# Kernel optimization log

Hardware: AMD Instinct MI355X
Metric: run time of the kernel (lower is better)

Reference implementation:

```python
import math
import jax, jax.numpy as jnp
import numpy as np

K = 30          # tokens per node (most recent links)
IN_CH = 100     # edge feature dim
HID = 100       # hidden channels
OUT_CH = 100    # output channels
TCH = 100       # temporal encoding dim
N = 50000       # num nodes
E = 800000      # num edges


def setup_inputs() -> dict:
    key = jax.random.key(0)
    ks = jax.random.split(key, 16)
    rn = lambda k, shape, s=0.05: (jax.random.normal(k, shape, jnp.float32) * s)
    return {
        'edge_attr': jax.random.normal(ks[0], (E, IN_CH), jnp.float32),
        'edge_time': jax.random.uniform(ks[1], (E,), jnp.float32),
        'node_batch': jax.random.randint(ks[2], (E,), 0, N, jnp.int32),
        'num_nodes': N,
        'head_w': rn(ks[3], (HID, TCH + IN_CH)), 'head_b': jnp.zeros((HID,), jnp.float32),
        'ln_t_g': jnp.ones((HID,), jnp.float32), 'ln_t_b': jnp.zeros((HID,), jnp.float32),
        'tok1_w': rn(ks[4], (K // 2, K)), 'tok1_b': jnp.zeros((K // 2,), jnp.float32),
        'tok2_w': rn(ks[5], (K, K // 2)), 'tok2_b': jnp.zeros((K,), jnp.float32),
        'ln_c_g': jnp.ones((HID,), jnp.float32), 'ln_c_b': jnp.zeros((HID,), jnp.float32),
        'ch1_w': rn(ks[6], (4 * HID, HID)), 'ch1_b': jnp.zeros((4 * HID,), jnp.float32),
        'ch2_w': rn(ks[7], (HID, 4 * HID)), 'ch2_b': jnp.zeros((HID,), jnp.float32),
        'ln_h_g': jnp.ones((HID,), jnp.float32), 'ln_h_b': jnp.zeros((HID,), jnp.float32),
        'out_w': rn(ks[8], (OUT_CH, HID)), 'out_b': jnp.zeros((OUT_CH,), jnp.float32),
    }


def _layer_norm(x, g, b, eps=1e-5):
    m = x.mean(-1, keepdims=True)
    v = ((x - m) ** 2).mean(-1, keepdims=True)
    return (x - m) * jax.lax.rsqrt(v + eps) * g + b


def _gelu(x):
    return jax.nn.gelu(x, approximate=False)  # torch default GELU is exact erf


def reference(edge_attr, edge_time, node_batch, num_nodes,
              head_w, head_b, ln_t_g, ln_t_b, tok1_w, tok1_b, tok2_w, tok2_b,
              ln_c_g, ln_c_b, ch1_w, ch1_b, ch2_w, ch2_b, ln_h_g, ln_h_b,
              out_w, out_b):
    # TemporalEncoding: cos(t * 1/sqrt(d)**linspace(0, sqrt(d), d))
    sqrt_d = math.sqrt(TCH)
    tw = 1.0 / sqrt_d ** jnp.linspace(0.0, sqrt_d, TCH)          # [TCH]
    time_info = jnp.cos(edge_time[:, None] * tw[None, :])        # [E, TCH]
    h = jnp.concatenate([time_info, edge_attr], axis=1) @ head_w.T + head_b  # [E, HID]

    # stable sort by node, take first K edges per node (PyG to_dense_batch)
    perm = jnp.argsort(node_batch)                               # stable
    nb = node_batch[perm]
    h = h[perm]
    pos = jnp.arange(nb.shape[0]) - jnp.searchsorted(nb, nb, side='left')
    idx = jnp.where(pos < K, nb * K + pos, num_nodes * K)        # overflow row -> garbage
    buf = jnp.zeros((num_nodes * K + 1, HID), h.dtype).at[idx].set(h)
    x = buf[:num_nodes * K].reshape(num_nodes, K, HID)           # [N, K, HID]

    # MLP-mixer (eval mode: dropout is identity)
    ht = _layer_norm(x, ln_t_g, ln_t_b).swapaxes(1, 2)           # [N, HID, K]
    ht = _gelu(ht @ tok1_w.T + tok1_b) @ tok2_w.T + tok2_b       # [N, HID, K]
    h_token = ht.swapaxes(1, 2) + x                              # [N, K, HID]

    hc = _layer_norm(h_token, ln_c_g, ln_c_b)
    hc = _gelu(hc @ ch1_w.T + ch1_b) @ ch2_w.T + ch2_b
    h_channel = hc + h_token                                     # [N, K, HID]

    t = _layer_norm(h_channel, ln_h_g, ln_h_b).mean(axis=1)      # [N, HID]
    return t @ out_w.T + out_b                                   # [N, OUT_CH]
```

## Files before the change

### kernel.cpp

```cpp
#include <hip/hip_runtime.h>
#include <math.h>

#define KTOK 30
#define HIDC 100
#define SBD() __builtin_amdgcn_sched_barrier(0x7F)
#define CEXP 0.33554829241286486f

typedef short s16x8 __attribute__((ext_vector_type(8)));
typedef float f32x4 __attribute__((ext_vector_type(4)));

__device__ __forceinline__ unsigned cvt_pk_bf16(float lo, float hi) {
    unsigned r;
    asm("v_cvt_pk_bf16_f32 %0, %1, %2" : "=v"(r) : "v"(lo), "v"(hi));
    return r;
}
__device__ __forceinline__ unsigned short cvt_bf16(float x) {
    unsigned r;
    asm("v_cvt_pk_bf16_f32 %0, %1, 0" : "=v"(r) : "v"(x));
    return (unsigned short)r;
}
__device__ __forceinline__ float bf2f(unsigned short h) {
    return __uint_as_float(((unsigned)h) << 16);
}
__device__ __forceinline__ float exp2_fast(float x) {
    float r;
    asm("v_exp_f32 %0, %1" : "=v"(r) : "v"(x));
    return r;
}
__device__ __forceinline__ float cos_rev(float rev) {
    float r;
    asm("v_cos_f32 %0, %1" : "=v"(r) : "v"(rev));
    return r;
}
__device__ __forceinline__ unsigned short f2bf(float f) {
    unsigned u = __float_as_uint(f);
    unsigned r = (u + 0x7FFFu + ((u >> 16) & 1u)) >> 16;
    return (unsigned short)r;
}
__device__ __forceinline__ float gelu(float x) {
    float xc = fminf(fmaxf(x, -2.75f), 2.75f);
    float s = xc * xc;
    float q = fmaf(s, -0.00059132f, 0.0132267f);
    q = fmaf(q, s, -0.122945f);
    q = fmaf(q, s, 0.793839f);
    float p = xc * q;
    float t = __builtin_amdgcn_fmed3f(p, -1.0f, 1.0f);
    float hx = 0.5f * x;
    return fmaf(hx, t, hx);
}

__global__ void count_kernel(const int* __restrict__ nb, int* __restrict__ cnt, int E) {
    int e = blockIdx.x * blockDim.x + threadIdx.x;
    if (e < E) atomicAdd(&cnt[nb[e]], 1);
}

__global__ void scanA_kernel(const int* __restrict__ cnt, int* __restrict__ offsets,
                             int* __restrict__ bsum, int n) {
    __shared__ int sd[1024];
    int tid = threadIdx.x;
    int i = blockIdx.x * 1024 + tid;
    int v = (i < n) ? cnt[i] : 0;
    sd[tid] = v;
    __syncthreads();
    for (int off = 1; off < 1024; off <<= 1) {
        int tv = (tid >= off) ? sd[tid - off] : 0;
        __syncthreads();
        sd[tid] += tv;
        __syncthreads();
    }
    if (i < n) offsets[i] = sd[tid] - v;
    if (tid == 1023) bsum[blockIdx.x] = sd[1023];
}

__global__ void scanB_kernel(int* __restrict__ bsum, int nbk) {
    if (threadIdx.x == 0 && blockIdx.x == 0) {
        int run = 0;
        for (int b = 0; b < nbk; b++) { int tv = bsum[b]; bsum[b] = run; run += tv; }
    }
}

__global__ void scanC_kernel(int* __restrict__ offsets, const int* __restrict__ bsum, int n) {
    int i = blockIdx.x * blockDim.x + threadIdx.x;
    if (i < n) offsets[i] += bsum[i >> 10];
}

__global__ void fill_kernel(const int* __restrict__ nb, int* __restrict__ cursor,
                            const int* __restrict__ offsets, int* __restrict__ order, int E) {
    int e = blockIdx.x * blockDim.x + threadIdx.x;
    if (e >= E) return;
    int n = nb[e];
    int p = atomicAdd(&cursor[n], 1);
    order[offsets[n] + p] = e;
}

__global__ void select_kernel(const int* __restrict__ cnt, const int* __restrict__ offsets,
                              const int* __restrict__ order, int* __restrict__ sel, int N) {
    int node = blockIdx.x * blockDim.x + threadIdx.x;
    if (node >= N) return;
    int c = cnt[node];
    int off = offsets[node];
    int top[KTOK];
    int m = 0;
    for (int i = 0; i < c; i++) {
        int e = order[off + i];
        if (m < KTOK) {
            int j = m++;
            while (j > 0 && top[j - 1] > e) { top[j] = top[j - 1]; j--; }
            top[j] = e;
        } else if (e < top[KTOK - 1]) {
            int j = KTOK - 1;
            while (j > 0 && top[j - 1] > e) { top[j] = top[j - 1]; j--; }
            top[j] = e;
        }
    }
    for (int p = 0; p < KTOK; p++) sel[node * KTOK + p] = (p < m) ? top[p] : -1;
}

__global__ void prep_kernel(const float* __restrict__ head_w, const float* __restrict__ ch1_w,
                            const float* __restrict__ ch2_w, const float* __restrict__ tok1_w,
                            const float* __restrict__ tok2_w,
                            const float* __restrict__ ln_c_g, const float* __restrict__ ln_c_b,
                            const float* __restrict__ ch1_b,
                            unsigned short* __restrict__ wf,
                            float* __restrict__ Sg1, float* __restrict__ b1p) {
    int i = blockIdx.x * blockDim.x + threadIdx.x;
    if (i >= 128000) {
        int h = i - 128000;
        if (h < 400) {
            float sg = 0.f, sb = 0.f;
            for (int k = 0; k < 100; k++) {
                float w = ch1_w[h * 100 + k];
                sg += w * ln_c_g[k];
                sb += w * ln_c_b[k];
            }
            Sg1[h] = sg;
            b1p[h] = sb + ch1_b[h];
        }
        return;
    }
    float val = 0.0f;
    if (i < 28672) {
        int ii = i & 7, lane = (i >> 3) & 63, rest = i >> 9;
        int nt = rest % 7, kt = rest / 7;
        int k = kt * 32 + ((lane >> 4) << 3) + ii;
        int n = nt * 16 + (lane & 15);
        if (k < 200 && n < 100) val = head_w[n * 200 + k];
    } else if (i < 79872) {
        int j = i - 28672;
        int ii = j & 7, lane = (j >> 3) & 63, rest = j >> 9;
        int nt = rest % 25, kt = rest / 25;
        int k = kt * 32 + ((lane >> 4) << 3) + ii;
        int n = nt * 16 + (lane & 15);
        if (k < 100) val = ch1_w[n * 100 + k] * ln_c_g[k];
    } else if (i < 126464) {
        int j = i - 79872;
        int ii = j & 7, lane = (j >> 3) & 63, rest = j >> 9;
        int nt = rest % 7, kt = rest / 7;
        int k = kt * 32 + ((lane >> 4) << 3) + ii;
        int n = nt * 16 + (lane & 15);
        if (k < 400 && n < 100) val = ch2_w[n * 400 + k];
    } else if (i < 126976) {
        int j = i - 126464;
        int ii = j & 7, lane = (j >> 3) & 63;
        int k = ((lane >> 4) << 3) + ii;
        int n = lane & 15;
        if (k < 30 && n < 15) val = tok1_w[n * 30 + k];
    } else {
        int j = i - 126976;
        int ii = j & 7, lane = (j >> 3) & 63, nt = j >> 9;
        int k = ((lane >> 4) << 3) + ii;
        int n = nt * 16 + (lane & 15);
        if (k < 15 && n < 30) val = tok2_w[n * 15 + k];
    }
    wf[i] = f2bf(val);
}

__global__ __launch_bounds__(128, 3) void fused_node_kernel(
    const float* __restrict__ edge_attr, const float* __restrict__ edge_time,
    const int* __restrict__ sel, const unsigned short* __restrict__ wf,
    const float* __restrict__ head_b,
    const float* __restrict__ ln_t_g, const float* __restrict__ ln_t_b,
    const float* __restrict__ tok1_b, const float* __restrict__ tok2_b,
    const float* __restrict__ Sg1, const float* __restrict__ b1p,
    const float* __restrict__ ch2_b,
    const float* __restrict__ ln_h_g, const float* __restrict__ ln_h_b,
    const float* __restrict__ out_w, const float* __restrict__ out_b,
    float* __restrict__ out, int N) {

    __shared__ __align__(16) unsigned short xb2[2][32 * 104];
    __shared__ __align__(16) unsigned short scr2[2][2560];

    const int t = threadIdx.x;
    const int wv = t >> 6, l = t & 63;
    const int g = l >> 4, c16 = l & 15;
    unsigned short* xbw = xb2[wv];
    unsigned short* scrw = scr2[wv];
    char* scrb = (char*)scrw;
    const int node = blockIdx.x * 2 + wv;

    const s16x8 zfrag = {0, 0, 0, 0, 0, 0, 0, 0};
    const f32x4 zacc = {0.f, 0.f, 0.f, 0.f};

    const s16x8* headWf_v = (const s16x8*)(wf);
    const s16x8* wg1f_v   = (const s16x8*)(wf + 28672);
    const s16x8* w2f_v    = (const s16x8*)(wf + 79872);
    const s16x8* tok1f_v  = (const s16x8*)(wf + 126464);
    const s16x8* tok2f_v  = (const s16x8*)(wf + 126976);

    int eload = (l < KTOK && node < N) ? sel[node * KTOK + l] : -1;
    unsigned long long vmask = __ballot(eload >= 0);
    int e0 = __shfl(eload, c16);
    int e1 = __shfl(eload, 16 + c16);
    float tt0 = (e0 >= 0) ? edge_time[e0] : 0.f;
    float tt1 = (e1 >= 0) ? edge_time[e1] : 0.f;
    const float INV2PI = 0.15915494309189535f;
    float Trev0 = tt0 * INV2PI, Trev1 = tt1 * INV2PI;
    const float* ab0 = edge_attr + (size_t)(e0 < 0 ? 0 : e0) * 100;
    const float* ab1 = edge_attr + (size_t)(e1 < 0 ? 0 : e1) * 100;

    f32x4 hacc[2][7];
    #pragma unroll
    for (int a = 0; a < 2; a++)
        #pragma unroll
        for (int c = 0; c < 7; c++) hacc[a][c] = zacc;

    #pragma unroll
    for (int kc = 0; kc < 4; kc++) {
        s16x8 af[2][2];
        #pragma unroll
        for (int mt = 0; mt < 2; mt++) {
            const float Trev = mt ? Trev1 : Trev0;
            const float* abm = mt ? ab1 : ab0;
            #pragma unroll
            for (int kk = 0; kk < 2; kk++) {
                const int kb0 = kc * 64 + kk * 32;
                if (kb0 >= 224) { af[mt][kk] = zfrag; continue; }
                union { s16x8 v; unsigned u[4]; } r;
                if (kb0 + 32 <= 100) {
                    float Ab = Trev * exp2_fast(-CEXP * (float)(kb0 + g * 8));
                    #pragma unroll
                    for (int i2 = 0; i2 < 8; i2 += 2) {
                        float v0 = cos_rev(Ab * exp2f(-CEXP * (float)i2));
                        float v1 = cos_rev(Ab * exp2f(-CEXP * (float)(i2 + 1)));
                        r.u[i2 >> 1] = cvt_pk_bf16(v0, v1);
                    }
                } else if (kb0 == 96) {
                    int aoff = kb0 + g * 8 - 100;
                    int ac = aoff < 0 ? 0 : aoff;
                    const float* ap = abm + ac;
                    float4 A0 = *(const float4*)ap;
                    float4 A1 = *(const float4*)(ap + 4);
                    float fa[8] = {A0.x, A0.y, A0.z, A0.w, A1.x, A1.y, A1.z, A1.w};
                    float Ab = Trev * exp2_fast(-CEXP * (float)(kb0 + g * 8));
                    #pragma unroll
                    for (int i2 = 0; i2 < 8; i2 += 2) {
                        float cc0 = cos_rev(Ab * exp2f(-CEXP * (float)i2));
                        float cc1 = cos_rev(Ab * exp2f(-CEXP * (float)(i2 + 1)));
                        float a0 = (g == 0) ? ((i2 >= 4) ? fa[(i2 >= 4) ? i2 - 4 : 0] : 0.f) : fa[i2];
                        float a1 = (g == 0) ? ((i2 + 1 >= 4) ? fa[(i2 + 1 >= 4) ? i2 - 3 : 0] : 0.f) : fa[i2 + 1];
                        int k0 = kb0 + g * 8 + i2;
                        float v0 = (k0 < 100) ? cc0 : a0;
                        float v1 = (k0 + 1 < 100) ? cc1 : a1;
                        r.u[i2 >> 1] = cvt_pk_bf16(v0, v1);
                    }
                } else if (kb0 <= 160) {
                    int ac = kb0 + g * 8 - 100;
                    const float* ap = abm + ac;
                    float4 A0 = *(const float4*)ap;
                    float4 A1 = *(const float4*)(ap + 4);
                    r.u[0] = cvt_pk_bf16(A0.x, A0.y);
                    r.u[1] = cvt_pk_bf16(A0.z, A0.w);
                    r.u[2] = cvt_pk_bf16(A1.x, A1.y);
                    r.u[3] = cvt_pk_bf16(A1.z, A1.w);
                } else {
                    int aoff = kb0 + g * 8 - 100;
                    int ac = aoff > 92 ? 92 : aoff;
                    const float* ap = abm + ac;
                    float4 A0 = *(const float4*)ap;
                    float4 A1 = *(const float4*)(ap + 4);
                    float fa[8] = {A0.x, A0.y, A0.z, A0.w, A1.x, A1.y, A1.z, A1.w};
                    #pragma unroll
                    for (int i2 = 0; i2 < 8; i2 += 2) {
                        int k0 = kb0 + g * 8 + i2;
                        float v0 = (k0 < 200) ? fa[i2] : 0.f;
                        float v1 = (k0 + 1 < 200) ? fa[i2 + 1] : 0.f;
                        r.u[i2 >> 1] = cvt_pk_bf16(v0, v1);
                    }
                }
                af[mt][kk] = r.v;
            }
        }
        #pragma unroll
        for (int nt = 0; nt < 7; nt++) {
            #pragma unroll
            for (int kk = 0; kk < 2; kk++) {
                if (kc == 3 && kk == 1) continue;
                s16x8 bf = headWf_v[((kc * 2 + kk) * 7 + nt) * 64 + l];
                #pragma unroll
                for (int mt = 0; mt < 2; mt++)
                    hacc[mt][nt] = __builtin_amdgcn_mfma_f32_16x16x32_bf16(af[mt][kk], bf, hacc[mt][nt], 0, 0, 0);
            }
        }
    }

    float g7[7], b7[7], hb7[7];
    #pragma unroll
    for (int nt = 0; nt < 7; nt++) {
        int cc = nt * 16 + c16; if (cc > 99) cc = 99;
        g7[nt] = ln_t_g[cc]; b7[nt] = ln_t_b[cc]; hb7[nt] = head_b[cc];
    }

    #pragma unroll
    for (int mt = 0; mt < 2; mt++)
        #pragma unroll
        for (int nt = 0; nt < 7; nt++)
            #pragma unroll
            for (int jj = 0; jj < 4; jj++) {
                int row = mt * 16 + g * 4 + jj;
                bool ok = (((vmask >> row) & 1ull) != 0) && (nt < 6 || c16 < 4);
                hacc[mt][nt][jj] = ok ? (hacc[mt][nt][jj] + hb7[nt]) : 0.f;
            }

    #pragma unroll
    for (int mt = 0; mt < 2; mt++)
        #pragma unroll
        for (int nt = 0; nt < 7; nt++)
            #pragma unroll
            for (int jj = 0; jj < 4; jj++) {
                int row = mt * 16 + g * 4 + jj;
                int col = nt * 16 + c16;
                if (col < 100)      xbw[row * 104 + col] = cvt_bf16(hacc[mt][nt][jj]);
                else if (col < 104) xbw[row * 104 + col] = 0;
            }

    float mv[2][4], rv[2][4];
    #pragma unroll
    for (int mt = 0; mt < 2; mt++)
        #pragma unroll
        for (int jj = 0; jj < 4; jj++) {
            float s = 0.f, s2 = 0.f;
            #pragma unroll
            for (int nt = 0; nt < 7; nt++) {
                float v = hacc[mt][nt][jj];
                s += v;
                s2 = fmaf(v, v, s2);
            }
            #pragma unroll
            for (int msk = 1; msk < 16; msk <<= 1) {
                s  += __shfl_xor(s, msk);
                s2 += __shfl_xor(s2, msk);
            }
            float m = s * 0.01f;
            float var = fmaxf(s2 * 0.01f - m * m, 0.f);
            mv[mt][jj] = m;
            rv[mt][jj] = rsqrtf(var + 1e-5f);
        }

    s16x8 av[7];
    #pragma unroll
    for (int nb = 0; nb < 2; nb++) {
        const int nt0 = nb ? 4 : 0;
        const int ntN = nb ? 3 : 4;
        #pragma unroll
        for (int nn = 0; nn < 4; nn++) {
            if (nn < ntN) {
                int nt = nt0 + nn;
                #pragma unroll
                for (int mt = 0; mt < 2; mt++) {
                    float h0 = fmaf((hacc[mt][nt][0] - mv[mt][0]) * rv[mt][0], g7[nt], b7[nt]);
                    float h1 = fmaf((hacc[mt][nt][1] - mv[mt][1]) * rv[mt][1], g7[nt], b7[nt]);
                    float h2 = fmaf((hacc[mt][nt][2] - mv[mt][2]) * rv[mt][2], g7[nt], b7[nt]);
                    float h3 = fmaf((hacc[mt][nt][3] - mv[mt][3]) * rv[mt][3], g7[nt], b7[nt]);
                    unsigned w0 = cvt_pk_bf16(h0, h1);
                    unsigned w1 = cvt_pk_bf16(h2, h3);
                    int ba = nn * 1024 + (c16 + 32 * mt + 16 * (g >> 1)) * 16 + 8 * (g & 1);
                    *(uint2*)(scrb + ba) = make_uint2(w0, w1);
                }
            }
        }
        SBD();
        #pragma unroll
        for (int nn = 0; nn < 4; nn++) {
            if (nn < ntN)
                av[nt0 + nn] = *(const s16x8*)(scrb + nn * 1024 + l * 16);
        }
        SBD();
    }

    {
        s16x8 b1 = tok1f_v[l];
        float bias1 = (c16 < 15) ? tok1_b[c16] : 0.f;
        #pragma unroll
        for (int mt7 = 0; mt7 < 7; mt7++) {
            f32x4 y = __builtin_amdgcn_mfma_f32_16x16x32_bf16(av[mt7], b1, zacc, 0, 0, 0);
            #pragma unroll
            for (int jj = 0; jj < 4; jj++) {
                int ba = mt7 * 512 + (((g * 4 + jj) + (c16 >> 3) * 16) * 16 + (c16 & 7) * 2);
                *(unsigned short*)(scrb + ba) = cvt_bf16(gelu(y[jj] + bias1));
            }
        }
        SBD();
        s16x8 b2a = tok2f_v[l];
        s16x8 b2b = tok2f_v[64 + l];
        float tb0 = tok2_b[c16];
        float tb1 = (c16 < 14) ? tok2_b[16 + c16] : 0.f;
        #pragma unroll
        for (int mt7 = 0; mt7 < 7; mt7++) {
            s16x8 a2 = zfrag;
            if (g < 2) a2 = *(const s16x8*)(scrb + mt7 * 512 + l * 16);
            f32x4 d0 = __builtin_amdgcn_mfma_f32_16x16x32_bf16(a2, b2a, zacc, 0, 0, 0);
            f32x4 d1 = __builtin_amdgcn_mfma_f32_16x16x32_bf16(a2, b2b, zacc, 0, 0, 0);
            #pragma unroll
            for (int jj = 0; jj < 4; jj++) {
                int chD = mt7 * 16 + g * 4 + jj;
                if (chD < 100) {
                    int idx0 = c16 * 104 + chD;
                    xbw[idx0] = cvt_bf16(bf2f(xbw[idx0]) + d0[jj] + tb0);
                    int tok1i = 16 + c16;
                    if (tok1i < 30) {
                        int idx1 = tok1i * 104 + chD;
                        xbw[idx1] = cvt_bf16(bf2f(xbw[idx1]) + d1[jj] + tb1);
                    }
                }
            }
        }
        SBD();
    }

    unsigned short* cbw0 = scrw;
    unsigned short* cbw1 = scrw + 1280;
    f32x4 acc2[2][7];
    {
        s16x8 a1f[2][4];
        #pragma unroll
        for (int mt = 0; mt < 2; mt++)
            #pragma unroll
            for (int kk = 0; kk < 4; kk++) {
                s16x8 a = zfrag;
                if (kk < 3 || g == 0)
                    a = *(const s16x8*)&xbw[(mt * 16 + c16) * 104 + kk * 32 + g * 8];
                a1f[mt][kk] = a;
            }
        SBD();

        float rs_r[2][4], rm_r[2][4];
        {
            float mA[2], rA[2];
            #pragma unroll
            for (int mt = 0; mt < 2; mt++) {
                float s = 0.f, s2 = 0.f;
                #pragma unroll
                for (int kk = 0; kk < 4; kk++)
                    #pragma unroll
                    for (int i = 0; i < 8; i++) {
                        float f = bf2f((unsigned short)a1f[mt][kk][i]);
                        s += f;
                        s2 = fmaf(f, f, s2);
                    }
                s  += __shfl_xor(s, 16);  s  += __shfl_xor(s, 32);
                s2 += __shfl_xor(s2, 16); s2 += __shfl_xor(s2, 32);
                float m = s * 0.01f;
                float var = fmaxf(s2 * 0.01f - m * m, 0.f);
                mA[mt] = m;
                rA[mt] = rsqrtf(var + 1e-5f);
            }
            #pragma unroll
            for (int mt = 0; mt < 2; mt++)
                #pragma unroll
                for (int jj = 0; jj < 4; jj++) {
                    int src = g * 4 + jj;
                    float mm = __shfl(mA[mt], src);
                    float rr = __shfl(rA[mt], src);
                    rs_r[mt][jj] = rr;
                    rm_r[mt][jj] = rr * mm;
                }
        }

        #pragma unroll
        for (int a = 0; a < 2; a++)
            #pragma unroll
            for (int c = 0; c < 7; c++) acc2[a][c] = zacc;

        for (int hc = 0; hc < 13; hc++) {
            unsigned short* cw = (hc & 1) ? cbw1 : cbw0;
            f32x4 acc1[2][2];
            float Sg[2], Bp[2];
            #pragma unroll
            for (int a = 0; a < 2; a++) { acc1[a][0] = zacc; acc1[a][1] = zacc; }
            #pragma unroll
            for (int ntl = 0; ntl < 2; ntl++) {
                int ntg = hc * 2 + ntl;
                if (ntg < 25) {
                    int h = ntg * 16 + c16;
                    Sg[ntl] = Sg1[h];
                    Bp[ntl] = b1p[h];
                    #pragma unroll
                    for (int kk = 0; kk < 4; kk++) {
                        s16x8 bfr = wg1f_v[(kk * 25 + ntg) * 64 + l];
                        #pragma unroll
                        for (int mt = 0; mt < 2; mt++)
                            acc1[mt][ntl] = __builtin_amdgcn_mfma_f32_16x16x32_bf16(a1f[mt][kk], bfr, acc1[mt][ntl], 0, 0, 0);
                    }
                }
            }
            #pragma unroll
            for (int ntl = 0; ntl < 2; ntl++) {
                int ntg = hc * 2 + ntl;
                if (ntg < 25) {
                    #pragma unroll
                    for (int mt = 0; mt < 2; mt++)
                        #pragma unroll
                        for (int jj = 0; jj < 4; jj++) {
                            int row = mt * 16 + g * 4 + jj;
                            float h1 = fmaf(rs_r[mt][jj], acc1[mt][ntl][jj],
                                            fmaf(-rm_r[mt][jj], Sg[ntl], Bp[ntl]));
                            cw[row * 40 + ntl * 16 + c16] = cvt_bf16(gelu(h1));
                        }
                }
            }
            SBD();
            if (hc > 0) {
                unsigned short* cr = (hc & 1) ? cbw0 : cbw1;
                s16x8 a2f[2];
                #pragma unroll
                for (int mt = 0; mt < 2; mt++)
                    a2f[mt] = *(const s16x8*)&cr[(mt * 16 + c16) * 40 + g * 8];
                #pragma unroll
                for (int nt2 = 0; nt2 < 7; nt2++) {
                    s16x8 b2f = w2f_v[((hc - 1) * 7 + nt2) * 64 + l];
                    #pragma unroll
                    for (int mt = 0; mt < 2; mt++)
                        acc2[mt][nt2] = __builtin_amdgcn_mfma_f32_16x16x32_bf16(a2f[mt], b2f, acc2[mt][nt2], 0, 0, 0);
                }
            }
            SBD();
        }
        {
            s16x8 a2f[2];
            #pragma unroll
            for (int mt = 0; mt < 2; mt++)
                a2f[mt] = *(const s16x8*)&cbw0[(mt * 16 + c16) * 40 + g * 8];
            #pragma unroll
            for (int nt2 = 0; nt2 < 7; nt2++) {
                s16x8 b2f = w2f_v[(12 * 7 + nt2) * 64 + l];
                #pragma unroll
                for (int mt = 0; mt < 2; mt++)
                    acc2[mt][nt2] = __builtin_amdgcn_mfma_f32_16x16x32_bf16(a2f[mt], b2f, acc2[mt][nt2], 0, 0, 0);
            }
            SBD();
        }
    }

    #pragma unroll
    for (int nt = 0; nt < 7; nt++) {
        int col = nt * 16 + c16;
        if (col < 100) {
            float bias = ch2_b[col];
            #pragma unroll
            for (int mt = 0; mt < 2; mt++)
                #pragma unroll
                for (int jj = 0; jj < 4; jj++) {
                    int row = mt * 16 + g * 4 + jj;
                    acc2[mt][nt][jj] += bias + bf2f(xbw[row * 104 + col]);
                }
        }
    }
    float m_[2][4], rs_[2][4];
    #pragma unroll
    for (int mt = 0; mt < 2; mt++)
        #pragma unroll
        for (int jj = 0; jj < 4; jj++) {
            float s = 0.f, s2 = 0.f;
            #pragma unroll
            for (int nt = 0; nt < 7; nt++) {
                float v = acc2[mt][nt][jj];
                s += v;
                s2 = fmaf(v, v, s2);
            }
            #pragma unroll
            for (int msk = 1; msk < 16; msk <<= 1) {
                s  += __shfl_xor(s, msk);
                s2 += __shfl_xor(s2, msk);
            }
            float m = s * 0.01f;
            float var = fmaxf(s2 * 0.01f - m * m, 0.f);
            m_[mt][jj]  = m;
            rs_[mt][jj] = rsqrtf(var + 1e-5f);
        }
    float cs[7];
    #pragma unroll
    for (int nt = 0; nt < 7; nt++) cs[nt] = 0.f;
    #pragma unroll
    for (int mt = 0; mt < 2; mt++)
        #pragma unroll
        for (int jj = 0; jj < 4; jj++) {
            int row = mt * 16 + g * 4 + jj;
            if (row < 30) {
                float m = m_[mt][jj], rs = rs_[mt][jj];
                #pragma unroll
                for (int nt = 0; nt < 7; nt++)
                    cs[nt] = fmaf(acc2[mt][nt][jj] - m, rs, cs[nt]);
            }
        }
    #pragma unroll
    for (int nt = 0; nt < 7; nt++) {
        cs[nt] += __shfl_xor(cs[nt], 16);
        cs[nt] += __shfl_xor(cs[nt], 32);
    }
    float* stF = (float*)scrw;
    if (g == 0) {
        #pragma unroll
        for (int nt = 0; nt < 7; nt++) {
            int col = nt * 16 + c16;
            if (col < 100)
                stF[col] = ln_h_g[col] * cs[nt] * (1.0f / 30.0f) + ln_h_b[col];
        }
    }
    SBD();
    #pragma unroll
    for (int p = 0; p < 2; p++) {
        int o = p * 64 + l;
        if (o < 100 && node < N) {
            float a = out_b[o];
            const float* wr = out_w + o * 100;
            #pragma unroll
            for (int c = 0; c < 100; c += 4) {
                float4 w4 = *(const float4*)(wr + c);
                f32x4 t4 = *(const f32x4*)&stF[c];
                a += w4.x * t4[0] + w4.y * t4[1] + w4.z * t4[2] + w4.w * t4[3];
            }
            out[(size_t)node * 100 + o] = a;
        }
    }
}


extern "C" void kernel_launch(void* const* d_in, const int* in_sizes, int n_in,
                              void* d_out, int out_size, void* d_ws, size_t ws_size,
                              hipStream_t stream) {
    const float* edge_attr  = (const float*)d_in[0];
    const float* edge_time  = (const float*)d_in[1];
    const int*   node_batch = (const int*)d_in[2];
    const float* head_w = (const float*)d_in[4];
    const float* head_b = (const float*)d_in[5];
    const float* ln_t_g = (const float*)d_in[6];
    const float* ln_t_b = (const float*)d_in[7];
    const float* tok1_w = (const float*)d_in[8];
    const float* tok1_b = (const float*)d_in[9];
    const float* tok2_w = (const float*)d_in[10];
    const float* tok2_b = (const float*)d_in[11];
    const float* ln_c_g = (const float*)d_in[12];
    const float* ln_c_b = (const float*)d_in[13];
    const float* ch1_w  = (const float*)d_in[14];
    const float* ch1_b  = (const float*)d_in[15];
    const float* ch2_w  = (const float*)d_in[16];
    const float* ch2_b  = (const float*)d_in[17];
    const float* ln_h_g = (const float*)d_in[18];
    const float* ln_h_b = (const float*)d_in[19];
    const float* out_w  = (const float*)d_in[20];
    const float* out_b  = (const float*)d_in[21];
    float* out = (float*)d_out;

    const int E = in_sizes[2];
    const int N = out_size / HIDC;

    int* cnt     = (int*)d_ws;
    int* cursor  = cnt + N;
    int* offsets = cursor + N;
    int* order   = offsets + N;
    int* sel     = order + E;
    unsigned short* wf = (unsigned short*)(sel + (size_t)N * KTOK);
    float* Sg1 = (float*)(wf + 128000);
    float* b1p = Sg1 + 400;
    int*   bsum = (int*)(b1p + 400);

    const int nbk = (N + 1023) / 1024;

    hipMemsetAsync(cnt, 0, (size_t)2 * N * sizeof(int), stream);
    count_kernel<<<(E + 255) / 256, 256, 0, stream>>>(node_batch, cnt, E);
    scanA_kernel<<<nbk, 1024, 0, stream>>>(cnt, offsets, bsum, N);
    scanB_kernel<<<1, 64, 0, stream>>>(bsum, nbk);
    scanC_kernel<<<(N + 255) / 256, 256, 0, stream>>>(offsets, bsum, N);
    fill_kernel<<<(E + 255) / 256, 256, 0, stream>>>(node_batch, cursor, offsets, order, E);
    select_kernel<<<(N + 255) / 256, 256, 0, stream>>>(cnt, offsets, order, sel, N);
    prep_kernel<<<502, 256, 0, stream>>>(head_w, ch1_w, ch2_w, tok1_w, tok2_w,
                                         ln_c_g, ln_c_b, ch1_b, wf, Sg1, b1p);
    fused_node_kernel<<<(N + 1) / 2, 128, 0, stream>>>(
        edge_attr, edge_time, sel, wf, head_b,
        ln_t_g, ln_t_b, tok1_b, tok2_b, Sg1, b1p,
        ch2_b, ln_h_g, ln_h_b, out_w, out_b, out, N);
}
```

Before: 1.054 ms.

## Accumulate token-mix output into register residual and compute channel LN stats in fp32

The token-mixing second GEMM is reorganized so tokens are the M dimension and channels the N dimension. Its MFMA results accumulate directly into the fp32 head-projection registers (hacc), which serve as the residual, instead of doing read-modify-write passes on the bf16 LDS tile. The channel LayerNorm statistics are then computed from those fp32 registers with lane shuffles, and the result is written to LDS once, replacing a bf16 reload plus a separate reduction. This removes a round of LDS traffic and a bf16 rounding step. In exchange, hacc stays live longer, which raises register pressure, and the weight prepack layout for tok2 changes.

After: 1.099 ms. 4.3% more time.

```diff
diff --git a/kernel.cpp b/kernel.cpp
--- a/kernel.cpp
+++ b/kernel.cpp
@@ -167,10 +167,10 @@
         if (k < 30 && n < 15) val = tok1_w[n * 30 + k];
     } else {
         int j = i - 126976;
-        int ii = j & 7, lane = (j >> 3) & 63, nt = j >> 9;
+        int ii = j & 7, lane = (j >> 3) & 63, mt = j >> 9;
+        int tok = mt * 16 + (lane & 15);
         int k = ((lane >> 4) << 3) + ii;
-        int n = nt * 16 + (lane & 15);
-        if (k < 15 && n < 30) val = tok2_w[n * 15 + k];
+        if (tok < 30 && k < 15) val = tok2_w[tok * 15 + k];
     }
     wf[i] = f2bf(val);
 }
@@ -205,7 +205,7 @@
     const s16x8* wg1f_v   = (const s16x8*)(wf + 28672);
     const s16x8* w2f_v    = (const s16x8*)(wf + 79872);
     const s16x8* tok1f_v  = (const s16x8*)(wf + 126464);
-    const s16x8* tok2f_v  = (const s16x8*)(wf + 126976);
+    const s16x8* tok2a_v  = (const s16x8*)(wf + 126976);
 
     int eload = (l < KTOK && node < N) ? sel[node * KTOK + l] : -1;
     unsigned long long vmask = __ballot(eload >= 0);
@@ -321,18 +321,6 @@
                 hacc[mt][nt][jj] = ok ? (hacc[mt][nt][jj] + hb7[nt]) : 0.f;
             }
 
-    #pragma unroll
-    for (int mt = 0; mt < 2; mt++)
-        #pragma unroll
-        for (int nt = 0; nt < 7; nt++)
-            #pragma unroll
-            for (int jj = 0; jj < 4; jj++) {
-                int row = mt * 16 + g * 4 + jj;
-                int col = nt * 16 + c16;
-                if (col < 100)      xbw[row * 104 + col] = cvt_bf16(hacc[mt][nt][jj]);
-                else if (col < 104) xbw[row * 104 + col] = 0;
-            }
-
     float mv[2][4], rv[2][4];
     #pragma unroll
     for (int mt = 0; mt < 2; mt++)
@@ -395,37 +383,76 @@
             f32x4 y = __builtin_amdgcn_mfma_f32_16x16x32_bf16(av[mt7], b1, zacc, 0, 0, 0);
             #pragma unroll
             for (int jj = 0; jj < 4; jj++) {
-                int ba = mt7 * 512 + (((g * 4 + jj) + (c16 >> 3) * 16) * 16 + (c16 & 7) * 2);
-                *(unsigned short*)(scrb + ba) = cvt_bf16(gelu(y[jj] + bias1));
+                int ch = mt7 * 16 + g * 4 + jj;
+                *(unsigned short*)(scrb + ch * 36 + c16 * 2) = cvt_bf16(gelu(y[jj] + bias1));
             }
         }
         SBD();
-        s16x8 b2a = tok2f_v[l];
-        s16x8 b2b = tok2f_v[64 + l];
-        float tb0 = tok2_b[c16];
-        float tb1 = (c16 < 14) ? tok2_b[16 + c16] : 0.f;
-        #pragma unroll
-        for (int mt7 = 0; mt7 < 7; mt7++) {
-            s16x8 a2 = zfrag;
-            if (g < 2) a2 = *(const s16x8*)(scrb + mt7 * 512 + l * 16);
-            f32x4 d0 = __builtin_amdgcn_mfma_f32_16x16x32_bf16(a2, b2a, zacc, 0, 0, 0);
-            f32x4 d1 = __builtin_amdgcn_mfma_f32_16x16x32_bf16(a2, b2b, zacc, 0, 0, 0);
+        #pragma unroll
+        for (int mt = 0; mt < 2; mt++) {
+            int row = mt * 16 + g * 4;
             #pragma unroll
             for (int jj = 0; jj < 4; jj++) {
-                int chD = mt7 * 16 + g * 4 + jj;
-                if (chD < 100) {
-                    int idx0 = c16 * 104 + chD;
-                    xbw[idx0] = cvt_bf16(bf2f(xbw[idx0]) + d0[jj] + tb0);
-                    int tok1i = 16 + c16;
-                    if (tok1i < 30) {
-                        int idx1 = tok1i * 104 + chD;
-                        xbw[idx1] = cvt_bf16(bf2f(xbw[idx1]) + d1[jj] + tb1);
-                    }
-                }
-            }
-        }
+                float tb = (row + jj < KTOK) ? tok2_b[row + jj] : 0.f;
+                #pragma unroll
+                for (int nt = 0; nt < 7; nt++) hacc[mt][nt][jj] += tb;
+            }
+        }
+        s16x8 a2t[2];
+        a2t[0] = tok2a_v[l];
+        a2t[1] = tok2a_v[64 + l];
+        #pragma unroll
+        for (int nt = 0; nt < 7; nt++) {
+            s16x8 by = zfrag;
+            if (g < 2) by = *(const s16x8*)(scrb + (nt * 16 + c16) * 36 + g * 16);
+            #pragma unroll
+            for (int mt = 0; mt < 2; mt++)
+                hacc[mt][nt] = __builtin_amdgcn_mfma_f32_16x16x32_bf16(a2t[mt], by, hacc[mt][nt], 0, 0, 0);
+        }
+        #pragma unroll
+        for (int mt = 0; mt < 2; mt++)
+            #pragma unroll
+            for (int jj = 0; jj < 4; jj++)
+                if (c16 >= 4) hacc[mt][6][jj] = 0.f;
         SBD();
     }
+
+    float rs_r[2][4], rm_r[2][4];
+    #pragma unroll
+    for (int mt = 0; mt < 2; mt++)
+        #pragma unroll
+        for (int jj = 0; jj < 4; jj++) {
+            float s = 0.f, s2 = 0.f;
+            #pragma unroll
+            for (int nt = 0; nt < 7; nt++) {
+                float v = hacc[mt][nt][jj];
+                s += v;
+                s2 = fmaf(v, v, s2);
+            }
+            #pragma unroll
+            for (int msk = 1; msk < 16; msk <<= 1) {
+                s  += __shfl_xor(s, msk);
+                s2 += __shfl_xor(s2, msk);
+            }
+            float m = s * 0.01f;
+            float var = fmaxf(s2 * 0.01f - m * m, 0.f);
+            float rr = rsqrtf(var + 1e-5f);
+            rs_r[mt][jj] = rr;
+            rm_r[mt][jj] = rr * m;
+        }
+
+    #pragma unroll
+    for (int mt = 0; mt < 2; mt++)
+        #pragma unroll
+        for (int nt = 0; nt < 7; nt++)
+            #pragma unroll
+            for (int jj = 0; jj < 4; jj++) {
+                int row = mt * 16 + g * 4 + jj;
+                int col = nt * 16 + c16;
+                if (col < 100)      xbw[row * 104 + col] = cvt_bf16(hacc[mt][nt][jj]);
+                else if (col < 104) xbw[row * 104 + col] = 0;
+            }
+    SBD();
 
     unsigned short* cbw0 = scrw;
     unsigned short* cbw1 = scrw + 1280;
@@ -442,39 +469,6 @@
                 a1f[mt][kk] = a;
             }
         SBD();
-
-        float rs_r[2][4], rm_r[2][4];
-        {
-            float mA[2], rA[2];
-            #pragma unroll
-            for (int mt = 0; mt < 2; mt++) {
-                float s = 0.f, s2 = 0.f;
-                #pragma unroll
-                for (int kk = 0; kk < 4; kk++)
-                    #pragma unroll
-                    for (int i = 0; i < 8; i++) {
-                        float f = bf2f((unsigned short)a1f[mt][kk][i]);
-                        s += f;
-                        s2 = fmaf(f, f, s2);
-                    }
-                s  += __shfl_xor(s, 16);  s  += __shfl_xor(s, 32);
-                s2 += __shfl_xor(s2, 16); s2 += __shfl_xor(s2, 32);
-                float m = s * 0.01f;
-                float var = fmaxf(s2 * 0.01f - m * m, 0.f);
-                mA[mt] = m;
-                rA[mt] = rsqrtf(var + 1e-5f);
-            }
-            #pragma unroll
-            for (int mt = 0; mt < 2; mt++)
-                #pragma unroll
-                for (int jj = 0; jj < 4; jj++) {
-                    int src = g * 4 + jj;
-                    float mm = __shfl(mA[mt], src);
-                    float rr = __shfl(rA[mt], src);
-                    rs_r[mt][jj] = rr;
-                    rm_r[mt][jj] = rr * mm;
-                }
-        }
 
         #pragma unroll
         for (int a = 0; a < 2; a++)
```

## Shrink LDS scratch and register pressure by fusing token-mix stages per tile

Applied to the files above, without the earlier changes.

Fuses the token-mixing LayerNorm, tok1 MFMA, GELU and tok2 MFMA into one loop over the 7 channel tiles, reusing a single small scratch region instead of holding 7 A-fragments in registers. It also drops the double-buffered hidden-chunk staging in the channel MLP, so each chunk is written, read back and consumed in the same iteration. Together this halves the per-wave scratch LDS and reduces live registers, aiming for higher occupancy. The cost is more sched barriers per tile and less overlap between the first and second channel GEMMs.

Measured after the change: 1.217 ms. 15.5% more time.

```diff
diff --git a/kernel.cpp b/kernel.cpp
--- a/kernel.cpp
+++ b/kernel.cpp
@@ -188,7 +188,7 @@
     float* __restrict__ out, int N) {
 
     __shared__ __align__(16) unsigned short xb2[2][32 * 104];
-    __shared__ __align__(16) unsigned short scr2[2][2560];
+    __shared__ __align__(16) unsigned short scr2[2][1280];
 
     const int t = threadIdx.x;
     const int wv = t >> 6, l = t & 63;
@@ -356,63 +356,44 @@
             rv[mt][jj] = rsqrtf(var + 1e-5f);
         }
 
-    s16x8 av[7];
-    #pragma unroll
-    for (int nb = 0; nb < 2; nb++) {
-        const int nt0 = nb ? 4 : 0;
-        const int ntN = nb ? 3 : 4;
-        #pragma unroll
-        for (int nn = 0; nn < 4; nn++) {
-            if (nn < ntN) {
-                int nt = nt0 + nn;
-                #pragma unroll
-                for (int mt = 0; mt < 2; mt++) {
-                    float h0 = fmaf((hacc[mt][nt][0] - mv[mt][0]) * rv[mt][0], g7[nt], b7[nt]);
-                    float h1 = fmaf((hacc[mt][nt][1] - mv[mt][1]) * rv[mt][1], g7[nt], b7[nt]);
-                    float h2 = fmaf((hacc[mt][nt][2] - mv[mt][2]) * rv[mt][2], g7[nt], b7[nt]);
-                    float h3 = fmaf((hacc[mt][nt][3] - mv[mt][3]) * rv[mt][3], g7[nt], b7[nt]);
-                    unsigned w0 = cvt_pk_bf16(h0, h1);
-                    unsigned w1 = cvt_pk_bf16(h2, h3);
-                    int ba = nn * 1024 + (c16 + 32 * mt + 16 * (g >> 1)) * 16 + 8 * (g & 1);
-                    *(uint2*)(scrb + ba) = make_uint2(w0, w1);
-                }
-            }
-        }
-        SBD();
-        #pragma unroll
-        for (int nn = 0; nn < 4; nn++) {
-            if (nn < ntN)
-                av[nt0 + nn] = *(const s16x8*)(scrb + nn * 1024 + l * 16);
-        }
-        SBD();
-    }
-
     {
         s16x8 b1 = tok1f_v[l];
         float bias1 = (c16 < 15) ? tok1_b[c16] : 0.f;
-        #pragma unroll
-        for (int mt7 = 0; mt7 < 7; mt7++) {
-            f32x4 y = __builtin_amdgcn_mfma_f32_16x16x32_bf16(av[mt7], b1, zacc, 0, 0, 0);
-            #pragma unroll
-            for (int jj = 0; jj < 4; jj++) {
-                int ba = mt7 * 512 + (((g * 4 + jj) + (c16 >> 3) * 16) * 16 + (c16 & 7) * 2);
-                *(unsigned short*)(scrb + ba) = cvt_bf16(gelu(y[jj] + bias1));
-            }
-        }
-        SBD();
         s16x8 b2a = tok2f_v[l];
         s16x8 b2b = tok2f_v[64 + l];
         float tb0 = tok2_b[c16];
         float tb1 = (c16 < 14) ? tok2_b[16 + c16] : 0.f;
         #pragma unroll
-        for (int mt7 = 0; mt7 < 7; mt7++) {
+        for (int nt = 0; nt < 7; nt++) {
+            #pragma unroll
+            for (int mt = 0; mt < 2; mt++) {
+                float h0 = fmaf((hacc[mt][nt][0] - mv[mt][0]) * rv[mt][0], g7[nt], b7[nt]);
+                float h1 = fmaf((hacc[mt][nt][1] - mv[mt][1]) * rv[mt][1], g7[nt], b7[nt]);
+                float h2 = fmaf((hacc[mt][nt][2] - mv[mt][2]) * rv[mt][2], g7[nt], b7[nt]);
+                float h3 = fmaf((hacc[mt][nt][3] - mv[mt][3]) * rv[mt][3], g7[nt], b7[nt]);
+                unsigned w0 = cvt_pk_bf16(h0, h1);
+                unsigned w1 = cvt_pk_bf16(h2, h3);
+                int ba = (c16 + 32 * mt + 16 * (g >> 1)) * 16 + 8 * (g & 1);
+                *(uint2*)(scrb + ba) = make_uint2(w0, w1);
+            }
+            SBD();
+            s16x8 av = *(const s16x8*)(scrb + l * 16);
+            SBD();
+            f32x4 y = __builtin_amdgcn_mfma_f32_16x16x32_bf16(av, b1, zacc, 0, 0, 0);
+            #pragma unroll
+            for (int jj = 0; jj < 4; jj++) {
+                int ba = 1024 + (((g * 4 + jj) + (c16 >> 3) * 16) * 16 + (c16 & 7) * 2);
+                *(unsigned short*)(scrb + ba) = cvt_bf16(gelu(y[jj] + bias1));
+            }
+            SBD();
             s16x8 a2 = zfrag;
-            if (g < 2) a2 = *(const s16x8*)(scrb + mt7 * 512 + l * 16);
+            if (g < 2) a2 = *(const s16x8*)(scrb + 1024 + l * 16);
+            SBD();
             f32x4 d0 = __builtin_amdgcn_mfma_f32_16x16x32_bf16(a2, b2a, zacc, 0, 0, 0);
             f32x4 d1 = __builtin_amdgcn_mfma_f32_16x16x32_bf16(a2, b2b, zacc, 0, 0, 0);
             #pragma unroll
             for (int jj = 0; jj < 4; jj++) {
-                int chD = mt7 * 16 + g * 4 + jj;
+                int chD = nt * 16 + g * 4 + jj;
                 if (chD < 100) {
                     int idx0 = c16 * 104 + chD;
                     xbw[idx0] = cvt_bf16(bf2f(xbw[idx0]) + d0[jj] + tb0);
@@ -423,12 +404,11 @@
                     }
                 }
             }
-        }
-        SBD();
-    }
-
-    unsigned short* cbw0 = scrw;
-    unsigned short* cbw1 = scrw + 1280;
+            SBD();
+        }
+    }
+
+    unsigned short* cbw = scrw;
     f32x4 acc2[2][7];
     {
         s16x8 a1f[2][4];
@@ -482,67 +462,42 @@
             for (int c = 0; c < 7; c++) acc2[a][c] = zacc;
 
         for (int hc = 0; hc < 13; hc++) {
-            unsigned short* cw = (hc & 1) ? cbw1 : cbw0;
-            f32x4 acc1[2][2];
-            float Sg[2], Bp[2];
-            #pragma unroll
-            for (int a = 0; a < 2; a++) { acc1[a][0] = zacc; acc1[a][1] = zacc; }
             #pragma unroll
             for (int ntl = 0; ntl < 2; ntl++) {
                 int ntg = hc * 2 + ntl;
                 if (ntg < 25) {
                     int h = ntg * 16 + c16;
-                    Sg[ntl] = Sg1[h];
-                    Bp[ntl] = b1p[h];
+                    float Sg = Sg1[h];
+                    float Bp = b1p[h];
+                    f32x4 acc1[2];
+                    acc1[0] = zacc; acc1[1] = zacc;
                     #pragma unroll
                     for (int kk = 0; kk < 4; kk++) {
                         s16x8 bfr = wg1f_v[(kk * 25 + ntg) * 64 + l];
                         #pragma unroll
                         for (int mt = 0; mt < 2; mt++)
-                            acc1[mt][ntl] = __builtin_amdgcn_mfma_f32_16x16x32_bf16(a1f[mt][kk], bfr, acc1[mt][ntl], 0, 0, 0);
+                            acc1[mt] = __builtin_amdgcn_mfma_f32_16x16x32_bf16(a1f[mt][kk], bfr, acc1[mt], 0, 0, 0);
                     }
-                }
-            }
-            #pragma unroll
-            for (int ntl = 0; ntl < 2; ntl++) {
-                int ntg = hc * 2 + ntl;
-                if (ntg < 25) {
                     #pragma unroll
                     for (int mt = 0; mt < 2; mt++)
                         #pragma unroll
                         for (int jj = 0; jj < 4; jj++) {
                             int row = mt * 16 + g * 4 + jj;
-                            float h1 = fmaf(rs_r[mt][jj], acc1[mt][ntl][jj],
-                                            fmaf(-rm_r[mt][jj], Sg[ntl], Bp[ntl]));
-                            cw[row * 40 + ntl * 16 + c16] = cvt_bf16(gelu(h1));
+                            float h1 = fmaf(rs_r[mt][jj], acc1[mt][jj],
+                                            fmaf(-rm_r[mt][jj], Sg, Bp));
+                            cbw[row * 40 + ntl * 16 + c16] = cvt_bf16(gelu(h1));
                         }
                 }
             }
             SBD();
-            if (hc > 0) {
-                unsigned short* cr = (hc & 1) ? cbw0 : cbw1;
-                s16x8 a2f[2];
-                #pragma unroll
-                for (int mt = 0; mt < 2; mt++)
-                    a2f[mt] = *(const s16x8*)&cr[(mt * 16 + c16) * 40 + g * 8];
-                #pragma unroll
-                for (int nt2 = 0; nt2 < 7; nt2++) {
-                    s16x8 b2f = w2f_v[((hc - 1) * 7 + nt2) * 64 + l];
-                    #pragma unroll
-                    for (int mt = 0; mt < 2; mt++)
-                        acc2[mt][nt2] = __builtin_amdgcn_mfma_f32_16x16x32_bf16(a2f[mt], b2f, acc2[mt][nt2], 0, 0, 0);
-                }
-            }
-            SBD();
-        }
-        {
             s16x8 a2f[2];
             #pragma unroll
             for (int mt = 0; mt < 2; mt++)
-                a2f[mt] = *(const s16x8*)&cbw0[(mt * 16 + c16) * 40 + g * 8];
+                a2f[mt] = *(const s16x8*)&cbw[(mt * 16 + c16) * 40 + g * 8];
+            SBD();
             #pragma unroll
             for (int nt2 = 0; nt2 < 7; nt2++) {
-                s16x8 b2f = w2f_v[(12 * 7 + nt2) * 64 + l];
+                s16x8 b2f = w2f_v[(hc * 7 + nt2) * 64 + l];
                 #pragma unroll
                 for (int mt = 0; mt < 2; mt++)
                     acc2[mt][nt2] = __builtin_amdgcn_mfma_f32_16x16x32_bf16(a2f[mt], b2f, acc2[mt][nt2], 0, 0, 0);
```
